# Kernel tuning notes

Hardware: AMD Instinct MI355X
Metric: run time of the kernel (lower is better)

Reference implementation:

```python
import jax, jax.numpy as jnp
import numpy as np

NUM_HEADS = 16
THETA = 10000.0


def _apply_rope(x, pos):
    # x: [b, h, t, d_k], pos: [t] int
    d = x.shape[-1]
    inv_freq = THETA ** (-jnp.arange(0, d, 2, dtype=jnp.float32) / d)  # [d/2]
    ang = pos.astype(jnp.float32)[:, None] * inv_freq                  # [t, d/2]
    cos, sin = jnp.cos(ang), jnp.sin(ang)
    x1, x2 = x[..., ::2], x[..., 1::2]
    r1 = x1 * cos - x2 * sin
    r2 = x1 * sin + x2 * cos
    return jnp.stack([r1, r2], axis=-1).reshape(x.shape)


def setup_inputs() -> dict:
    key = jax.random.key(0)
    k1, k2, k3 = jax.random.split(key, 3)
    b, t, dm = 4, 2048, 2048
    in_features = jax.random.normal(k1, (b, t, dm), dtype=jnp.float32)
    token_positions = jnp.arange(t, dtype=jnp.int64)
    W_qkv = jax.random.normal(k2, (3 * dm, dm), dtype=jnp.float32) * 0.02
    W_o = jax.random.normal(k3, (dm, dm), dtype=jnp.float32) * 0.02
    return {"in_features": in_features, "token_positions": token_positions,
            "W_qkv": W_qkv, "W_o": W_o}


def reference(in_features, token_positions, W_qkv, W_o):
    b, t, dm = in_features.shape
    h = NUM_HEADS
    dk = dm // h
    # fused QKV projection (Linear: y = x W^T)
    qkv = in_features @ W_qkv.T                       # [b, t, 3*dm]
    q, k, v = jnp.split(qkv, 3, axis=-1)
    def to_heads(x):
        return x.reshape(b, t, h, dk).transpose(0, 2, 1, 3)  # [b, h, t, dk]
    q, k, v = to_heads(q), to_heads(k), to_heads(v)
    q = _apply_rope(q, token_positions)
    k = _apply_rope(k, token_positions)
    # causal SDPA
    scale = 1.0 / np.sqrt(dk).astype(np.float32)
    scores = jnp.einsum('bhqd,bhkd->bhqk', q, k) * scale
    causal = jnp.tril(jnp.ones((t, t), dtype=bool))
    scores = jnp.where(causal, scores, jnp.finfo(scores.dtype).min)
    attn = jax.nn.softmax(scores, axis=-1)
    out = jnp.einsum('bhqk,bhkd->bhqd', attn, v)      # [b, h, t, dk]
    out = out.transpose(0, 2, 1, 3).reshape(b, t, dm)
    return out @ W_o.T
```

## Files before the change

### kernel.cpp

```cpp
#include <hip/hip_runtime.h>

typedef unsigned short u16;
typedef __attribute__((ext_vector_type(8))) short s8v;
typedef __attribute__((ext_vector_type(8))) __bf16 bf8;
typedef __attribute__((ext_vector_type(4))) float f4v;

#define GLB(p) ((const __attribute__((address_space(1))) void*)(p))
#define LDS(p) ((__attribute__((address_space(3))) void*)(p))

static __device__ __forceinline__ float b2f(u16 u) {
    union { unsigned int i; float f; } v; v.i = ((unsigned int)u) << 16; return v.f;
}
static __device__ __forceinline__ u16 f2b(float f) {
    union { float f; unsigned int i; } v; v.f = f;
    v.i += 0x7fffu + ((v.i >> 16) & 1u);
    return (u16)(v.i >> 16);
}

__global__ __launch_bounds__(256) void k_conv(const float* __restrict__ X,
                                              const float* __restrict__ Wq,
                                              const float* __restrict__ Wo,
                                              u16* __restrict__ Xb,
                                              u16* __restrict__ Wqb,
                                              u16* __restrict__ Wob) {
    int i = blockIdx.x * 256 + threadIdx.x;
    const float* in; u16* out; int off;
    if (i < 4194304)      { in = X;  out = Xb;  off = i; }
    else if (i < 7340032) { in = Wq; out = Wqb; off = i - 4194304; }
    else                  { in = Wo; out = Wob; off = i - 7340032; }
    float4 v = ((const float4*)in)[off];
    union { u16 u[4]; unsigned long long ll; } o;
    o.u[0] = f2b(v.x); o.u[1] = f2b(v.y); o.u[2] = f2b(v.z); o.u[3] = f2b(v.w);
    ((unsigned long long*)out)[off] = o.ll;
}

template<int MODE>
__global__ __launch_bounds__(512, 2) void k_gemm_bt(
    const u16* __restrict__ A, const u16* __restrict__ B,
    int K, int N, int gx,
    u16* __restrict__ Qb, u16* __restrict__ Kb, u16* __restrict__ Vt,
    float* __restrict__ Cf, const int* __restrict__ pos)
{
    extern __shared__ __align__(16) u16 Ls[];

    const int t    = threadIdx.x;
    const int lane = t & 63;
    const int wid  = t >> 6;
    const int wm = wid >> 2, wn = wid & 3;
    const int la = lane & 15, lb = lane >> 4;

    const int bid = (int)blockIdx.x;
    const int id2 = (bid & 7) * ((int)gridDim.x >> 3) + (bid >> 3);
    const int bx = id2 % gx, by = id2 / gx;
    const long arow0 = (long)by * 256;
    const long brow0 = (long)bx * 256;

    const int sr = t >> 3;
    const int sg = (t & 7) ^ (sr & 7);
    const u16* Asrc = A + (arow0 + sr) * (long)K + sg * 8;
    const u16* Bsrc = B + (brow0 + sr) * (long)K + sg * 8;
    const long K64 = 64 * (long)K, K128 = 128 * (long)K;
    u16* ldst = Ls + t * 8;

#define STG(q_, op_, h_, kt_) do {                                              \
        const u16* s_ = ((op_) ? Bsrc : Asrc) + (h_) * K128 + (long)(kt_) * 64; \
        u16* d_ = ldst + (q_) * 32768 + (op_) * 16384 + (h_) * 8192;            \
        __builtin_amdgcn_global_load_lds(GLB(s_),       LDS(d_),        16, 0, 0); \
        __builtin_amdgcn_global_load_lds(GLB(s_ + K64), LDS(d_ + 4096), 16, 0, 0); \
    } while (0)
#define RD(off) (*(const bf8*)(Ls + (off)))

    f4v acc[8][4];
#pragma unroll
    for (int m = 0; m < 8; m++)
#pragma unroll
        for (int n = 0; n < 4; n++) acc[m][n] = (f4v){0.f, 0.f, 0.f, 0.f};

    const int r7 = la & 7;
    const int gA0 = (lb ^ r7) * 8;
    const int gA1 = ((lb ^ r7) ^ 4) * 8;
    const int aRow = wm * 8192 + la * 64;
    const int bRow = 16384 + (wn >> 1) * 8192 + ((wn & 1) * 64 + la) * 64;

    const int NKT = K >> 6;
    STG(0, 0, 0, 0); STG(0, 0, 1, 0); STG(0, 1, 0, 0); STG(0, 1, 1, 0);
    asm volatile("s_waitcnt vmcnt(0)" ::: "memory");
    __builtin_amdgcn_s_barrier();

    for (int X = 0; X < NKT; ++X) {
        const int D = (X & 1) << 15;
        const int q = (X + 1) & 1;
        const int S = (X + 1 < NKT) ? X + 1 : NKT - 1;
        bf8 aR[4][2], b0[2][2], b1[2][2];

#pragma unroll
        for (int mi = 0; mi < 4; mi++) {
            aR[mi][0] = RD(D + aRow + mi * 1024 + gA0);
            aR[mi][1] = RD(D + aRow + mi * 1024 + gA1);
        }
#pragma unroll
        for (int nl = 0; nl < 2; nl++) {
            b0[nl][0] = RD(D + bRow + nl * 1024 + gA0);
            b0[nl][1] = RD(D + bRow + nl * 1024 + gA1);
        }
        STG(q, 0, 0, S); STG(q, 0, 1, S); STG(q, 1, 0, S); STG(q, 1, 1, S);
        __builtin_amdgcn_s_barrier();
        __builtin_amdgcn_s_setprio(1);
#pragma unroll
        for (int mi = 0; mi < 4; mi++)
#pragma unroll
            for (int nl = 0; nl < 2; nl++) {
                acc[mi][nl] = __builtin_amdgcn_mfma_f32_16x16x32_bf16(aR[mi][0], b0[nl][0], acc[mi][nl], 0, 0, 0);
                acc[mi][nl] = __builtin_amdgcn_mfma_f32_16x16x32_bf16(aR[mi][1], b0[nl][1], acc[mi][nl], 0, 0, 0);
            }
        __builtin_amdgcn_s_setprio(0);

#pragma unroll
        for (int nl = 0; nl < 2; nl++) {
            b1[nl][0] = RD(D + bRow + (2 + nl) * 1024 + gA0);
            b1[nl][1] = RD(D + bRow + (2 + nl) * 1024 + gA1);
        }
        __builtin_amdgcn_s_barrier();
        __builtin_amdgcn_s_setprio(1);
#pragma unroll
        for (int mi = 0; mi < 4; mi++)
#pragma unroll
            for (int nl = 0; nl < 2; nl++) {
                acc[mi][2 + nl] = __builtin_amdgcn_mfma_f32_16x16x32_bf16(aR[mi][0], b1[nl][0], acc[mi][2 + nl], 0, 0, 0);
                acc[mi][2 + nl] = __builtin_amdgcn_mfma_f32_16x16x32_bf16(aR[mi][1], b1[nl][1], acc[mi][2 + nl], 0, 0, 0);
            }
        __builtin_amdgcn_s_setprio(0);

#pragma unroll
        for (int mi = 0; mi < 4; mi++) {
            aR[mi][0] = RD(D + aRow + (4 + mi) * 1024 + gA0);
            aR[mi][1] = RD(D + aRow + (4 + mi) * 1024 + gA1);
        }
        __builtin_amdgcn_s_barrier();
        __builtin_amdgcn_s_setprio(1);
#pragma unroll
        for (int mi = 0; mi < 4; mi++)
#pragma unroll
            for (int nl = 0; nl < 2; nl++) {
                acc[4 + mi][2 + nl] = __builtin_amdgcn_mfma_f32_16x16x32_bf16(aR[mi][0], b1[nl][0], acc[4 + mi][2 + nl], 0, 0, 0);
                acc[4 + mi][2 + nl] = __builtin_amdgcn_mfma_f32_16x16x32_bf16(aR[mi][1], b1[nl][1], acc[4 + mi][2 + nl], 0, 0, 0);
            }
        __builtin_amdgcn_s_setprio(0);

        asm volatile("s_waitcnt vmcnt(0)" ::: "memory");
        __builtin_amdgcn_s_barrier();
        __builtin_amdgcn_s_setprio(1);
#pragma unroll
        for (int mi = 0; mi < 4; mi++)
#pragma unroll
            for (int nl = 0; nl < 2; nl++) {
                acc[4 + mi][nl] = __builtin_amdgcn_mfma_f32_16x16x32_bf16(aR[mi][0], b0[nl][0], acc[4 + mi][nl], 0, 0, 0);
                acc[4 + mi][nl] = __builtin_amdgcn_mfma_f32_16x16x32_bf16(aR[mi][1], b0[nl][1], acc[4 + mi][nl], 0, 0, 0);
            }
        __builtin_amdgcn_s_setprio(0);
    }
#undef STG
#undef RD

    if (MODE == 1) {
#pragma unroll
        for (int mi = 0; mi < 8; mi++)
#pragma unroll
            for (int ni = 0; ni < 4; ni++) {
                const long grow0 = arow0 + wm * 128 + mi * 16 + lb * 4;
                const int  gcol  = (int)brow0 + wn * 64 + ni * 16 + la;
#pragma unroll
                for (int i = 0; i < 4; i++)
                    Cf[(grow0 + i) * (long)N + gcol] = acc[mi][ni][i];
            }
        return;
    }

    __syncthreads();
    const int part = (int)(brow0 >> 11);
    const int colp = (int)brow0 & 2047;
    const int h0   = colp >> 7;
    const int bidx = (int)(arow0 >> 11);
    const int t0   = (int)arow0 & 2047;

    if (part == 2) {
#pragma unroll
        for (int mi = 0; mi < 8; mi++)
#pragma unroll
            for (int ni = 0; ni < 4; ni++) {
                const int tlb = wm * 128 + mi * 16 + lb * 4;
                const int dl  = wn * 64 + ni * 16 + la;
#pragma unroll
                for (int i2 = 0; i2 < 2; i2++) {
                    unsigned int pk = (unsigned int)f2b(acc[mi][ni][i2 * 2])
                                    | ((unsigned int)f2b(acc[mi][ni][i2 * 2 + 1]) << 16);
                    *(unsigned int*)(Ls + dl * 264 + tlb + i2 * 2) = pk;
                }
            }
        __syncthreads();
#pragma unroll
        for (int j = 0; j < 16; j++) {
            const int dl = j * 16 + wid * 2 + (lane >> 5);
            const int c  = lane & 31;
            bf8 v = *(const bf8*)(Ls + dl * 264 + c * 8);
            const long bh = (long)(bidx * 16 + h0 + (dl >> 7));
            *(bf8*)(Vt + (bh << 18) + ((long)(dl & 127) << 11) + t0 + c * 8) = v;
        }
    } else {
        u16* dst = (part == 0) ? Qb : Kb;
#pragma unroll
        for (int mi = 0; mi < 8; mi++)
#pragma unroll
            for (int ni = 0; ni < 4; ni++) {
                const int tlb = wm * 128 + mi * 16 + lb * 4;
                const int dl  = wn * 64 + ni * 16 + la;
#pragma unroll
                for (int i = 0; i < 4; i++)
                    Ls[(tlb + i) * 264 + dl] = f2b(acc[mi][ni][i]);
            }
        __syncthreads();
        const int c = t & 15;
        float invf[4];
#pragma unroll
        for (int p2 = 0; p2 < 4; p2++)
            invf[p2] = exp2f((float)(c * 4 + p2) * -0.20762050593046014f);
#pragma unroll
        for (int j = 0; j < 16; j++) {
            const int R  = j * 32 + (t >> 4);
            const int tl = R >> 1, hh = R & 1;
            s8v v = *(const s8v*)(Ls + tl * 264 + hh * 128 + c * 8);
            const float pf = (float)pos[t0 + tl];
            union { u16 u[8]; s8v v; } ov;
#pragma unroll
            for (int p2 = 0; p2 < 4; p2++) {
                float x1 = b2f((u16)v[2 * p2]);
                float x2 = b2f((u16)v[2 * p2 + 1]);
                float sn, cs;
                __sincosf(pf * invf[p2], &sn, &cs);
                ov.u[2 * p2]     = f2b(x1 * cs - x2 * sn);
                ov.u[2 * p2 + 1] = f2b(x1 * sn + x2 * cs);
            }
            const long bh = (long)(bidx * 16 + h0 + hh);
            *(s8v*)(dst + ((bh << 11) + t0 + tl) * 128 + c * 8) = ov.v;
        }
    }
}

__global__ __launch_bounds__(256) void k_attn(const u16* __restrict__ Qb,
                                              const u16* __restrict__ Kb,
                                              const u16* __restrict__ Vt,
                                              u16* __restrict__ Ob)
{
    extern __shared__ __align__(16) u16 Sm[];
    u16* KsD = Sm;
    u16* VsD = Sm + 16384;
    u16* PlD = Sm + 32768;

    const int tid  = threadIdx.x;
    const int lane = tid & 63;
    const int w    = tid >> 6;
    const int la = lane & 15, lb = lane >> 4;
    const int qg = 15 - ((int)blockIdx.x >> 6);
    const int bh = blockIdx.x & 63;
    const long base = (long)bh << 18;
    const int qt = qg * 4 + w;
    const int q0 = qt * 32;
    const int n32 = qt + 1;
    const int NT = qg * 2 + 2;
    const float scale = 0.08838834764831845f;

    bf8 qf[2][4];
#pragma unroll
    for (int m = 0; m < 2; m++)
#pragma unroll
        for (int kb = 0; kb < 4; kb++)
            qf[m][kb] = *(const bf8*)(Qb + base + (long)(q0 + m * 16 + la) * 128 + kb * 32 + lb * 8);

    f4v o[2][8];
#pragma unroll
    for (int m = 0; m < 2; m++)
#pragma unroll
        for (int n = 0; n < 8; n++) o[m][n] = (f4v){0.f, 0.f, 0.f, 0.f};
    float lst[2][4];
#pragma unroll
    for (int m = 0; m < 2; m++)
#pragma unroll
        for (int i = 0; i < 4; i++) lst[m][i] = 0.f;

    char* Pb = (char*)(PlD + w * 1024);

    const int krow = tid >> 4;
    const int kgr  = (tid & 15) ^ (krow & 7);
    const int vrow = tid >> 3;
    const int vgr  = (tid & 7) ^ (vrow & 7);

#define STAGE(buf, jt_) do {                                                         \
        const int kv0_ = (jt_) * 64;                                                \
        _Pragma("unroll")                                                           \
        for (int i_ = 0; i_ < 4; i_++) {                                            \
            __builtin_amdgcn_global_load_lds(                                       \
                GLB(Kb + base + (long)(kv0_ + i_ * 16 + krow) * 128 + kgr * 8),     \
                LDS(KsD + (buf) * 8192 + i_ * 2048 + tid * 8), 16, 0, 0);           \
            __builtin_amdgcn_global_load_lds(                                       \
                GLB(Vt + base + (long)(i_ * 32 + vrow) * 2048 + kv0_ + vgr * 8),    \
                LDS(VsD + (buf) * 8192 + i_ * 2048 + tid * 8), 16, 0, 0);           \
        }                                                                           \
    } while (0)

    STAGE(0, 0);

    for (int jt = 0; jt < NT; ++jt) {
        const int buf = jt & 1;
        asm volatile("s_waitcnt vmcnt(0)" ::: "memory");
        __builtin_amdgcn_s_barrier();
        if (jt + 1 < NT) STAGE(buf ^ 1, jt + 1);

        const u16* KsB = KsD + buf * 8192;
        const u16* VsB = VsD + buf * 8192;

#pragma unroll
        for (int h = 0; h < 2; h++) {
            const int j32 = jt * 2 + h;
            if (j32 < n32) {
                f4v s[2][2];
                s[0][0] = s[0][1] = s[1][0] = s[1][1] = (f4v){0.f, 0.f, 0.f, 0.f};
#pragma unroll
                for (int n = 0; n < 2; n++) {
                    const int rr = h * 32 + n * 16 + la;
#pragma unroll
                    for (int kb = 0; kb < 4; kb++) {
                        bf8 kf = *(const bf8*)(KsB + rr * 128 + (((kb * 4 + lb) ^ (la & 7)) * 8));
                        s[0][n] = __builtin_amdgcn_mfma_f32_16x16x32_bf16(qf[0][kb], kf, s[0][n], 0, 0, 0);
                        s[1][n] = __builtin_amdgcn_mfma_f32_16x16x32_bf16(qf[1][kb], kf, s[1][n], 0, 0, 0);
                    }
                }

                bf8 vf[8];
#pragma unroll
                for (int nO = 0; nO < 8; nO++) {
                    const int rv = nO * 16 + la;
                    vf[nO] = *(const bf8*)(VsB + rv * 64 + (((h * 4 + lb) ^ (la & 7)) * 8));
                }

                const bool diag = (j32 == qt);
                float p[2][2][4];
#pragma unroll
                for (int m = 0; m < 2; m++)
#pragma unroll
                    for (int n = 0; n < 2; n++)
#pragma unroll
                        for (int i = 0; i < 4; i++) {
                            float v = __expf(fmaf(s[m][n][i], scale, -8.0f));
                            if (diag && (n * 16 + la) > (m * 16 + lb * 4 + i)) v = 0.f;
                            p[m][n][i] = v;
                            lst[m][i] += v;
                        }

#pragma unroll
                for (int m = 0; m < 2; m++)
#pragma unroll
                    for (int n = 0; n < 2; n++)
#pragma unroll
                        for (int i = 0; i < 4; i++) {
                            const int row = m * 16 + lb * 4 + i;
                            const int colb = (n * 16 + la) * 2;
                            *(u16*)(Pb + row * 64 + (colb ^ (lb << 4))) = f2b(p[m][n][i]);
                        }
                bf8 pa[2];
#pragma unroll
                for (int am = 0; am < 2; am++) {
                    const int row = am * 16 + la;
                    pa[am] = *(const bf8*)(Pb + row * 64 + ((lb * 16) ^ ((la & 12) << 2)));
                }
#pragma unroll
                for (int nO = 0; nO < 8; nO++) {
                    o[0][nO] = __builtin_amdgcn_mfma_f32_16x16x32_bf16(pa[0], vf[nO], o[0][nO], 0, 0, 0);
                    o[1][nO] = __builtin_amdgcn_mfma_f32_16x16x32_bf16(pa[1], vf[nO], o[1][nO], 0, 0, 0);
                }
            }
        }
    }
#undef STAGE

    float linv[2][4];
#pragma unroll
    for (int m = 0; m < 2; m++)
#pragma unroll
        for (int i = 0; i < 4; i++) {
            float l = lst[m][i];
            l += __shfl_xor(l, 1);
            l += __shfl_xor(l, 2);
            l += __shfl_xor(l, 4);
            l += __shfl_xor(l, 8);
            linv[m][i] = 1.0f / l;
        }

    const int b = bh >> 4, h = bh & 15;
#pragma unroll
    for (int m = 0; m < 2; m++)
#pragma unroll
        for (int nO = 0; nO < 8; nO++)
#pragma unroll
            for (int i = 0; i < 4; i++) {
                const int row = q0 + m * 16 + lb * 4 + i;
                const int d = nO * 16 + la;
                Ob[((long)(b * 2048 + row) << 11) + h * 128 + d] = f2b(o[m][nO][i] * linv[m][i]);
            }
}

extern "C" void kernel_launch(void* const* d_in, const int* in_sizes, int n_in,
                              void* d_out, int out_size, void* d_ws, size_t ws_size,
                              hipStream_t stream)
{
    const float* X    = (const float*)d_in[0];
    const int*   pos  = (const int*)d_in[1];
    const float* Wqkv = (const float*)d_in[2];
    const float* Wo   = (const float*)d_in[3];
    float* out = (float*)d_out;

    char* ws = (char*)d_ws;
    u16* Xb    = (u16*)(ws + 0);
    u16* Wqkvb = (u16*)(ws + 33554432);
    u16* Wob   = (u16*)(ws + 58720256);
    u16* Qb    = (u16*)(ws + 67108864);
    u16* Kb    = (u16*)(ws + 100663296);
    u16* Vt    = (u16*)(ws + 134217728);
    u16* Ob    = (u16*)(ws + 167772160);

    k_conv<<<32768, 256, 0, stream>>>(X, Wqkv, Wo, Xb, Wqkvb, Wob);
    k_gemm_bt<0><<<768, 512, 135168, stream>>>(Xb, Wqkvb, 2048, 6144, 24, Qb, Kb, Vt, nullptr, pos);
    k_attn<<<1024, 256, 73728, stream>>>(Qb, Kb, Vt, Ob);
    k_gemm_bt<1><<<256, 512, 131072, stream>>>(Ob, Wob, 2048, 2048, 8, nullptr, nullptr, nullptr, out, nullptr);
}
```

Measured before the change: 394.3 us.

## Widen attention warps to 64 query rows and specialize diagonal tile masking

Each wave now processes 64 query rows instead of 32, so a block covers 256 rows and the grid halves to 512 blocks. Every K/V fragment read from LDS feeds twice as many MFMAs, and fewer blocks re-stream the same K/V. The diagonal tile is split into a masked path that skips the fully masked upper row-blocks, while off-diagonal tiles run without mask checks. In exchange, accumulator register pressure doubles (launch_bounds 256,2), there are fewer blocks to spread across CUs, and causal load imbalance gets coarser.

```diff
diff --git a/kernel.cpp b/kernel.cpp
--- a/kernel.cpp
+++ b/kernel.cpp
@@ -246,10 +246,10 @@
     }
 }
 
-__global__ __launch_bounds__(256) void k_attn(const u16* __restrict__ Qb,
-                                              const u16* __restrict__ Kb,
-                                              const u16* __restrict__ Vt,
-                                              u16* __restrict__ Ob)
+__global__ __launch_bounds__(256, 2) void k_attn(const u16* __restrict__ Qb,
+                                                 const u16* __restrict__ Kb,
+                                                 const u16* __restrict__ Vt,
+                                                 u16* __restrict__ Ob)
 {
     extern __shared__ __align__(16) u16 Sm[];
     u16* KsD = Sm;
@@ -260,34 +260,34 @@
     const int lane = tid & 63;
     const int w    = tid >> 6;
     const int la = lane & 15, lb = lane >> 4;
-    const int qg = 15 - ((int)blockIdx.x >> 6);
+    const int qg = 7 - ((int)blockIdx.x >> 6);
     const int bh = blockIdx.x & 63;
     const long base = (long)bh << 18;
     const int qt = qg * 4 + w;
-    const int q0 = qt * 32;
-    const int n32 = qt + 1;
-    const int NT = qg * 2 + 2;
+    const int q0 = qt * 64;
+    const int n64 = qt + 1;
+    const int NT = qg * 4 + 4;
     const float scale = 0.08838834764831845f;
 
-    bf8 qf[2][4];
-#pragma unroll
-    for (int m = 0; m < 2; m++)
+    bf8 qf[4][4];
+#pragma unroll
+    for (int m = 0; m < 4; m++)
 #pragma unroll
         for (int kb = 0; kb < 4; kb++)
             qf[m][kb] = *(const bf8*)(Qb + base + (long)(q0 + m * 16 + la) * 128 + kb * 32 + lb * 8);
 
-    f4v o[2][8];
-#pragma unroll
-    for (int m = 0; m < 2; m++)
+    f4v o[4][8];
+#pragma unroll
+    for (int m = 0; m < 4; m++)
 #pragma unroll
         for (int n = 0; n < 8; n++) o[m][n] = (f4v){0.f, 0.f, 0.f, 0.f};
-    float lst[2][4];
-#pragma unroll
-    for (int m = 0; m < 2; m++)
+    float lst[4][4];
+#pragma unroll
+    for (int m = 0; m < 4; m++)
 #pragma unroll
         for (int i = 0; i < 4; i++) lst[m][i] = 0.f;
 
-    char* Pb = (char*)(PlD + w * 1024);
+    char* Pb2 = (char*)(PlD + w * 2048);
 
     const int krow = tid >> 4;
     const int kgr  = (tid & 15) ^ (krow & 7);
@@ -307,6 +307,44 @@
         }                                                                           \
     } while (0)
 
+#define TILEBODY(MLO, DIAG, MOFF) do {                                               \
+    f4v s[4][2];                                                                     \
+    _Pragma("unroll") for (int m = MLO; m < 4; m++) {                                \
+        s[m][0] = (f4v){0.f, 0.f, 0.f, 0.f}; s[m][1] = (f4v){0.f, 0.f, 0.f, 0.f};    \
+    }                                                                                \
+    _Pragma("unroll") for (int n = 0; n < 2; n++) {                                  \
+        const int rr = h * 32 + n * 16 + la;                                         \
+        _Pragma("unroll") for (int kb = 0; kb < 4; kb++) {                           \
+            bf8 kf = *(const bf8*)(KsB + rr * 128 + (((kb * 4 + lb) ^ (la & 7)) * 8)); \
+            _Pragma("unroll") for (int m = MLO; m < 4; m++)                          \
+                s[m][n] = __builtin_amdgcn_mfma_f32_16x16x32_bf16(qf[m][kb], kf, s[m][n], 0, 0, 0); \
+        }                                                                            \
+    }                                                                                \
+    bf8 vf[8];                                                                       \
+    _Pragma("unroll") for (int nO = 0; nO < 8; nO++) {                               \
+        const int rv = nO * 16 + la;                                                 \
+        vf[nO] = *(const bf8*)(VsB + rv * 64 + (((h * 4 + lb) ^ (la & 7)) * 8));     \
+    }                                                                                \
+    _Pragma("unroll") for (int m = MLO; m < 4; m++)                                  \
+        _Pragma("unroll") for (int n = 0; n < 2; n++)                                \
+            _Pragma("unroll") for (int i = 0; i < 4; i++) {                          \
+                float v = __expf(fmaf(s[m][n][i], scale, -8.0f));                    \
+                if (DIAG && (n * 16 + la) > ((m - MOFF) * 16 + lb * 4 + i)) v = 0.f; \
+                lst[m][i] += v;                                                      \
+                const int row = m * 16 + lb * 4 + i;                                 \
+                const int colb = (n * 16 + la) * 2;                                  \
+                *(u16*)(Pb2 + row * 64 + (colb ^ (lb << 4))) = f2b(v);               \
+            }                                                                        \
+    bf8 pa[4];                                                                       \
+    _Pragma("unroll") for (int am = MLO; am < 4; am++) {                             \
+        const int row = am * 16 + la;                                                \
+        pa[am] = *(const bf8*)(Pb2 + row * 64 + ((lb * 16) ^ ((la & 12) << 2)));     \
+    }                                                                                \
+    _Pragma("unroll") for (int nO = 0; nO < 8; nO++)                                 \
+        _Pragma("unroll") for (int am = MLO; am < 4; am++)                           \
+            o[am][nO] = __builtin_amdgcn_mfma_f32_16x16x32_bf16(pa[am], vf[nO], o[am][nO], 0, 0, 0); \
+} while (0)
+
     STAGE(0, 0);
 
     for (int jt = 0; jt < NT; ++jt) {
@@ -315,76 +353,25 @@
         __builtin_amdgcn_s_barrier();
         if (jt + 1 < NT) STAGE(buf ^ 1, jt + 1);
 
-        const u16* KsB = KsD + buf * 8192;
-        const u16* VsB = VsD + buf * 8192;
-
-#pragma unroll
-        for (int h = 0; h < 2; h++) {
-            const int j32 = jt * 2 + h;
-            if (j32 < n32) {
-                f4v s[2][2];
-                s[0][0] = s[0][1] = s[1][0] = s[1][1] = (f4v){0.f, 0.f, 0.f, 0.f};
-#pragma unroll
-                for (int n = 0; n < 2; n++) {
-                    const int rr = h * 32 + n * 16 + la;
-#pragma unroll
-                    for (int kb = 0; kb < 4; kb++) {
-                        bf8 kf = *(const bf8*)(KsB + rr * 128 + (((kb * 4 + lb) ^ (la & 7)) * 8));
-                        s[0][n] = __builtin_amdgcn_mfma_f32_16x16x32_bf16(qf[0][kb], kf, s[0][n], 0, 0, 0);
-                        s[1][n] = __builtin_amdgcn_mfma_f32_16x16x32_bf16(qf[1][kb], kf, s[1][n], 0, 0, 0);
-                    }
-                }
-
-                bf8 vf[8];
-#pragma unroll
-                for (int nO = 0; nO < 8; nO++) {
-                    const int rv = nO * 16 + la;
-                    vf[nO] = *(const bf8*)(VsB + rv * 64 + (((h * 4 + lb) ^ (la & 7)) * 8));
-                }
-
-                const bool diag = (j32 == qt);
-                float p[2][2][4];
-#pragma unroll
-                for (int m = 0; m < 2; m++)
-#pragma unroll
-                    for (int n = 0; n < 2; n++)
-#pragma unroll
-                        for (int i = 0; i < 4; i++) {
-                            float v = __expf(fmaf(s[m][n][i], scale, -8.0f));
-                            if (diag && (n * 16 + la) > (m * 16 + lb * 4 + i)) v = 0.f;
-                            p[m][n][i] = v;
-                            lst[m][i] += v;
-                        }
-
-#pragma unroll
-                for (int m = 0; m < 2; m++)
-#pragma unroll
-                    for (int n = 0; n < 2; n++)
-#pragma unroll
-                        for (int i = 0; i < 4; i++) {
-                            const int row = m * 16 + lb * 4 + i;
-                            const int colb = (n * 16 + la) * 2;
-                            *(u16*)(Pb + row * 64 + (colb ^ (lb << 4))) = f2b(p[m][n][i]);
-                        }
-                bf8 pa[2];
-#pragma unroll
-                for (int am = 0; am < 2; am++) {
-                    const int row = am * 16 + la;
-                    pa[am] = *(const bf8*)(Pb + row * 64 + ((lb * 16) ^ ((la & 12) << 2)));
-                }
-#pragma unroll
-                for (int nO = 0; nO < 8; nO++) {
-                    o[0][nO] = __builtin_amdgcn_mfma_f32_16x16x32_bf16(pa[0], vf[nO], o[0][nO], 0, 0, 0);
-                    o[1][nO] = __builtin_amdgcn_mfma_f32_16x16x32_bf16(pa[1], vf[nO], o[1][nO], 0, 0, 0);
-                }
+        if (jt < n64) {
+            const u16* KsB = KsD + buf * 8192;
+            const u16* VsB = VsD + buf * 8192;
+            const bool lastT = (jt == n64 - 1);
+            if (!lastT) {
+#pragma unroll
+                for (int h = 0; h < 2; h++) TILEBODY(0, false, 0);
+            } else {
+                { const int h = 0; TILEBODY(0, true, 0); }
+                { const int h = 1; TILEBODY(2, true, 2); }
             }
         }
     }
 #undef STAGE
-
-    float linv[2][4];
-#pragma unroll
-    for (int m = 0; m < 2; m++)
+#undef TILEBODY
+
+    float linv[4][4];
+#pragma unroll
+    for (int m = 0; m < 4; m++)
 #pragma unroll
         for (int i = 0; i < 4; i++) {
             float l = lst[m][i];
@@ -395,16 +382,16 @@
             linv[m][i] = 1.0f / l;
         }
 
-    const int b = bh >> 4, h = bh & 15;
-#pragma unroll
-    for (int m = 0; m < 2; m++)
+    const int b = bh >> 4, hd = bh & 15;
+#pragma unroll
+    for (int m = 0; m < 4; m++)
 #pragma unroll
         for (int nO = 0; nO < 8; nO++)
 #pragma unroll
             for (int i = 0; i < 4; i++) {
                 const int row = q0 + m * 16 + lb * 4 + i;
                 const int d = nO * 16 + la;
-                Ob[((long)(b * 2048 + row) << 11) + h * 128 + d] = f2b(o[m][nO][i] * linv[m][i]);
+                Ob[((long)(b * 2048 + row) << 11) + hd * 128 + d] = f2b(o[m][nO][i] * linv[m][i]);
             }
 }
 
@@ -429,6 +416,6 @@
 
     k_conv<<<32768, 256, 0, stream>>>(X, Wqkv, Wo, Xb, Wqkvb, Wob);
     k_gemm_bt<0><<<768, 512, 135168, stream>>>(Xb, Wqkvb, 2048, 6144, 24, Qb, Kb, Vt, nullptr, pos);
-    k_attn<<<1024, 256, 73728, stream>>>(Qb, Kb, Vt, Ob);
+    k_attn<<<512, 256, 81920, stream>>>(Qb, Kb, Vt, Ob);
     k_gemm_bt<1><<<256, 512, 131072, stream>>>(Ob, Wob, 2048, 2048, 8, nullptr, nullptr, nullptr, out, nullptr);
 }
```

Measured after the change: 766.2 us. 94.3% more time.
